# Optimization experiments

Measured on AMD Instinct MI355X. Metric: run time of the kernel, lower is better.

The kernel has to match this reference:

```python
import jax, jax.numpy as jnp
import numpy as np

LAMBDA_COORD = 5.0
LAMBDA_OBJ = 1.0
LAMBDA_NOOBJ = 0.5
LAMBDA_CLS = 1.0
EPS = 1e-07

B, N, M, NUM_CLASSES = 32, 25200, 200, 80


def setup_inputs() -> dict:
    key = jax.random.key(0)
    k1, k2, k3, k4, k5 = jax.random.split(key, 5)
    pred_bbox = jax.random.normal(k1, (B, N, 4), dtype=jnp.float32)
    pred_obj = jax.random.normal(k2, (B, N), dtype=jnp.float32)
    pred_cls = jax.random.normal(k3, (B, N, NUM_CLASSES), dtype=jnp.float32)
    gt_boxes = jax.random.uniform(k4, (B, M, 4), dtype=jnp.float32)
    gt_labels = jax.random.randint(k5, (B, M), 0, NUM_CLASSES, dtype=jnp.int64 if jax.config.jax_enable_x64 else jnp.int32)
    return {"pred_bbox": pred_bbox, "pred_obj": pred_obj, "pred_cls": pred_cls,
            "gt_boxes": gt_boxes, "gt_labels": gt_labels}


def _corners(boxes):
    # boxes: [..., 4] in (cx, cy, w, h)
    cx, cy, w, h = boxes[..., 0], boxes[..., 1], boxes[..., 2], boxes[..., 3]
    return cx - w / 2, cy - h / 2, cx + w / 2, cy + h / 2


def giou_loss(pred_boxes, target_boxes):
    px1, py1, px2, py2 = _corners(pred_boxes)
    tx1, ty1, tx2, ty2 = _corners(target_boxes)
    ix1 = jnp.maximum(px1, tx1)
    iy1 = jnp.maximum(py1, ty1)
    ix2 = jnp.minimum(px2, tx2)
    iy2 = jnp.minimum(py2, ty2)
    inter = jnp.clip(ix2 - ix1, 0) * jnp.clip(iy2 - iy1, 0)
    union = (px2 - px1) * (py2 - py1) + (tx2 - tx1) * (ty2 - ty1) - inter
    iou = inter / (union + EPS)
    ex1 = jnp.minimum(px1, tx1)
    ey1 = jnp.minimum(py1, ty1)
    ex2 = jnp.maximum(px2, tx2)
    ey2 = jnp.maximum(py2, ty2)
    enclose = (ex2 - ex1) * (ey2 - ey1)
    return 1.0 - (iou - (enclose - union) / (enclose + EPS))


def reference(pred_bbox, pred_obj, pred_cls, gt_boxes, gt_labels):
    m = gt_boxes.shape[1]  # obj_mask[b,:m] = True (static), anchor n < m matches gt n
    # bbox GIoU loss over positives
    loss_bbox = giou_loss(pred_bbox[:, :m], gt_boxes).mean() * LAMBDA_COORD
    # objectness BCE-with-logits: positives target 1, negatives target 0
    pos_logits = pred_obj[:, :m]
    neg_logits = pred_obj[:, m:]
    loss_obj_pos = jnp.mean(jax.nn.softplus(-pos_logits)) * LAMBDA_OBJ
    loss_obj_neg = jnp.mean(jax.nn.softplus(neg_logits)) * LAMBDA_NOOBJ
    loss_obj = loss_obj_pos + loss_obj_neg
    # classification cross-entropy over positives
    logits = pred_cls[:, :m]                       # [B, M, C]
    logp = jax.nn.log_softmax(logits, axis=-1)
    nll = -jnp.take_along_axis(logp, gt_labels[..., None].astype(jnp.int32), axis=-1)[..., 0]
    loss_cls = nll.mean() * LAMBDA_CLS
    total = loss_bbox + loss_obj + loss_cls
    # [detection_loss, bbox_loss, obj_loss, cls_loss]
    return jnp.stack([total, loss_bbox, loss_obj, loss_cls])
```

## Files before the change

kernel.cpp:

```cpp
#include <hip/hip_runtime.h>

#define BB 32
#define NN 25200
#define MM 200
#define CC 80

constexpr float EPSF = 1e-7f;
constexpr float L_COORD = 5.0f;
constexpr float L_NOOBJ = 0.5f;

constexpr int ITEMS_GIOU = BB * MM;
constexpr int ITEMS_CLS  = BB * MM;
constexpr int ITEMS_OBJ  = BB * NN;
constexpr int ITEMS_TOTAL = ITEMS_GIOU + ITEMS_CLS + ITEMS_OBJ;

constexpr int BLOCK = 256;
constexpr int GRID  = 1024;

__device__ __forceinline__ float softplus_f(float x) {
    return fmaxf(x, 0.0f) + log1pf(expf(-fabsf(x)));
}

__global__ __launch_bounds__(BLOCK)
void detloss_kernel(const float* __restrict__ pred_bbox,
                    const float* __restrict__ pred_obj,
                    const float* __restrict__ pred_cls,
                    const float* __restrict__ gt_boxes,
                    const int*   __restrict__ gt_labels,
                    float* __restrict__ out,
                    float* __restrict__ ws)
{
    float s_bbox = 0.0f, s_obj = 0.0f, s_cls = 0.0f;

    const int stride = GRID * BLOCK;
    for (int i = blockIdx.x * BLOCK + threadIdx.x; i < ITEMS_TOTAL; i += stride) {
        if (i < ITEMS_GIOU) {
            const int b = i / MM, m = i - b * MM;
            const float4 p = *(const float4*)(pred_bbox + ((size_t)b * NN + m) * 4);
            const float4 t = *(const float4*)(gt_boxes + (size_t)i * 4);
            const float px1 = p.x - p.z * 0.5f, py1 = p.y - p.w * 0.5f;
            const float px2 = p.x + p.z * 0.5f, py2 = p.y + p.w * 0.5f;
            const float tx1 = t.x - t.z * 0.5f, ty1 = t.y - t.w * 0.5f;
            const float tx2 = t.x + t.z * 0.5f, ty2 = t.y + t.w * 0.5f;
            const float ix1 = fmaxf(px1, tx1), iy1 = fmaxf(py1, ty1);
            const float ix2 = fminf(px2, tx2), iy2 = fminf(py2, ty2);
            const float inter = fmaxf(ix2 - ix1, 0.0f) * fmaxf(iy2 - iy1, 0.0f);
            const float uni = (px2 - px1) * (py2 - py1)
                            + (tx2 - tx1) * (ty2 - ty1) - inter;
            const float iou = inter / (uni + EPSF);
            const float ex1 = fminf(px1, tx1), ey1 = fminf(py1, ty1);
            const float ex2 = fmaxf(px2, tx2), ey2 = fmaxf(py2, ty2);
            const float enc = (ex2 - ex1) * (ey2 - ey1);
            s_bbox += 1.0f - (iou - (enc - uni) / (enc + EPSF));
        } else if (i < ITEMS_GIOU + ITEMS_CLS) {
            const int r = i - ITEMS_GIOU;
            const int b = r / MM, m = r - b * MM;
            const float* row = pred_cls + ((size_t)b * NN + m) * CC;
            float mx = -INFINITY;
            float v[CC];
            #pragma unroll 4
            for (int c = 0; c < CC; ++c) { v[c] = row[c]; mx = fmaxf(mx, v[c]); }
            float se = 0.0f;
            #pragma unroll 4
            for (int c = 0; c < CC; ++c) se += expf(v[c] - mx);
            const float lse = mx + logf(se);
            const int lbl = gt_labels[r];
            s_cls += lse - v[lbl];
        } else {
            const int e = i - (ITEMS_GIOU + ITEMS_CLS);
            const int n = e % NN;
            const float x = pred_obj[e];
            if (n < MM) s_obj += softplus_f(-x) * (1.0f / (float)(BB * MM));
            else        s_obj += softplus_f(x) * (L_NOOBJ / (float)(BB * (NN - MM)));
        }
    }

    #pragma unroll
    for (int off = 32; off > 0; off >>= 1) {
        s_bbox += __shfl_down(s_bbox, off, 64);
        s_obj  += __shfl_down(s_obj,  off, 64);
        s_cls  += __shfl_down(s_cls,  off, 64);
    }

    __shared__ float red[3][BLOCK / 64];
    const int wave = threadIdx.x >> 6;
    const int lane = threadIdx.x & 63;
    if (lane == 0) {
        red[0][wave] = s_bbox;
        red[1][wave] = s_obj;
        red[2][wave] = s_cls;
    }
    __syncthreads();

    if (threadIdx.x == 0) {
        float tb = 0.0f, to = 0.0f, tc = 0.0f;
        #pragma unroll
        for (int w = 0; w < BLOCK / 64; ++w) {
            tb += red[0][w]; to += red[1][w]; tc += red[2][w];
        }
        atomicAdd(&ws[0], tb);
        atomicAdd(&ws[1], to);
        atomicAdd(&ws[2], tc);
        __threadfence();
        const unsigned ticket = atomicAdd((unsigned*)&ws[3], 1u);
        if (ticket == (unsigned)(gridDim.x - 1)) {
            const float sb = atomicAdd(&ws[0], 0.0f);
            const float so = atomicAdd(&ws[1], 0.0f);
            const float sc = atomicAdd(&ws[2], 0.0f);
            const float loss_bbox = sb * (L_COORD / (float)(BB * MM));
            const float loss_obj  = so;
            const float loss_cls  = sc * (1.0f / (float)(BB * MM));
            out[0] = loss_bbox + loss_obj + loss_cls;
            out[1] = loss_bbox;
            out[2] = loss_obj;
            out[3] = loss_cls;
        }
    }
}

extern "C" void kernel_launch(void* const* d_in, const int* in_sizes, int n_in,
                              void* d_out, int out_size, void* d_ws, size_t ws_size,
                              hipStream_t stream) {
    const float* pred_bbox = (const float*)d_in[0];
    const float* pred_obj  = (const float*)d_in[1];
    const float* pred_cls  = (const float*)d_in[2];
    const float* gt_boxes  = (const float*)d_in[3];
    const int*   gt_labels = (const int*)d_in[4];
    float* out = (float*)d_out;
    float* ws  = (float*)d_ws;

    hipMemsetAsync(ws, 0, 4 * sizeof(float), stream);
    detloss_kernel<<<GRID, BLOCK, 0, stream>>>(pred_bbox, pred_obj, pred_cls,
                                               gt_boxes, gt_labels, out, ws);
}
```

Measured before the change: 365.9 us.

## Split class rows across 16 lanes, vectorize objectness loads, two-pass reduction

```diff
diff --git a/kernel.cpp b/kernel.cpp
--- a/kernel.cpp
+++ b/kernel.cpp
@@ -7,34 +7,34 @@
 
 constexpr float EPSF = 1e-7f;
 constexpr float L_COORD = 5.0f;
-constexpr float L_NOOBJ = 0.5f;
-
-constexpr int ITEMS_GIOU = BB * MM;
-constexpr int ITEMS_CLS  = BB * MM;
-constexpr int ITEMS_OBJ  = BB * NN;
-constexpr int ITEMS_TOTAL = ITEMS_GIOU + ITEMS_CLS + ITEMS_OBJ;
 
 constexpr int BLOCK = 256;
 constexpr int GRID  = 1024;
 
+constexpr int R_GIOU = BB * MM;
+constexpr int R_CLS  = R_GIOU + BB * MM * 16;
+constexpr int R_OBJ  = R_CLS + (BB * NN) / 4;
+
+constexpr float W_POS = 1.0f / (float)(BB * MM);
+constexpr float W_NEG = 0.5f / (float)(BB * (NN - MM));
+
 __device__ __forceinline__ float softplus_f(float x) {
-    return fmaxf(x, 0.0f) + log1pf(expf(-fabsf(x)));
+    return fmaxf(x, 0.0f) + __logf(1.0f + __expf(-fabsf(x)));
 }
 
 __global__ __launch_bounds__(BLOCK)
-void detloss_kernel(const float* __restrict__ pred_bbox,
-                    const float* __restrict__ pred_obj,
-                    const float* __restrict__ pred_cls,
-                    const float* __restrict__ gt_boxes,
-                    const int*   __restrict__ gt_labels,
-                    float* __restrict__ out,
-                    float* __restrict__ ws)
+void detloss_partials(const float* __restrict__ pred_bbox,
+                      const float* __restrict__ pred_obj,
+                      const float* __restrict__ pred_cls,
+                      const float* __restrict__ gt_boxes,
+                      const int*   __restrict__ gt_labels,
+                      float* __restrict__ ws)
 {
     float s_bbox = 0.0f, s_obj = 0.0f, s_cls = 0.0f;
 
     const int stride = GRID * BLOCK;
-    for (int i = blockIdx.x * BLOCK + threadIdx.x; i < ITEMS_TOTAL; i += stride) {
-        if (i < ITEMS_GIOU) {
+    for (int i = blockIdx.x * BLOCK + threadIdx.x; i < R_OBJ; i += stride) {
+        if (i < R_GIOU) {
             const int b = i / MM, m = i - b * MM;
             const float4 p = *(const float4*)(pred_bbox + ((size_t)b * NN + m) * 4);
             const float4 t = *(const float4*)(gt_boxes + (size_t)i * 4);
@@ -52,26 +52,43 @@
             const float ex2 = fmaxf(px2, tx2), ey2 = fmaxf(py2, ty2);
             const float enc = (ex2 - ex1) * (ey2 - ey1);
             s_bbox += 1.0f - (iou - (enc - uni) / (enc + EPSF));
-        } else if (i < ITEMS_GIOU + ITEMS_CLS) {
-            const int r = i - ITEMS_GIOU;
+        } else if (i < R_CLS) {
+            const int q   = i - R_GIOU;
+            const int r   = q >> 4;
+            const int sub = q & 15;
             const int b = r / MM, m = r - b * MM;
             const float* row = pred_cls + ((size_t)b * NN + m) * CC;
-            float mx = -INFINITY;
-            float v[CC];
-            #pragma unroll 4
-            for (int c = 0; c < CC; ++c) { v[c] = row[c]; mx = fmaxf(mx, v[c]); }
-            float se = 0.0f;
-            #pragma unroll 4
-            for (int c = 0; c < CC; ++c) se += expf(v[c] - mx);
-            const float lse = mx + logf(se);
-            const int lbl = gt_labels[r];
-            s_cls += lse - v[lbl];
+            float v0 = row[sub];
+            float v1 = row[sub + 16];
+            float v2 = row[sub + 32];
+            float v3 = row[sub + 48];
+            float v4 = row[sub + 64];
+            float mx = fmaxf(fmaxf(fmaxf(v0, v1), fmaxf(v2, v3)), v4);
+            #pragma unroll
+            for (int off = 1; off < 16; off <<= 1)
+                mx = fmaxf(mx, __shfl_xor(mx, off, 16));
+            float se = __expf(v0 - mx) + __expf(v1 - mx) + __expf(v2 - mx)
+                     + __expf(v3 - mx) + __expf(v4 - mx);
+            #pragma unroll
+            for (int off = 1; off < 16; off <<= 1)
+                se += __shfl_xor(se, off, 16);
+            if (sub == 0) {
+                const float lse = mx + __logf(se);
+                const int lbl = gt_labels[r];
+                s_cls += lse - row[lbl];
+            }
         } else {
-            const int e = i - (ITEMS_GIOU + ITEMS_CLS);
+            const int o = i - R_CLS;
+            const int e = o * 4;
             const int n = e % NN;
-            const float x = pred_obj[e];
-            if (n < MM) s_obj += softplus_f(-x) * (1.0f / (float)(BB * MM));
-            else        s_obj += softplus_f(x) * (L_NOOBJ / (float)(BB * (NN - MM)));
+            const float4 x = *(const float4*)(pred_obj + e);
+            if (n < MM) {
+                s_obj += W_POS * (softplus_f(-x.x) + softplus_f(-x.y)
+                                + softplus_f(-x.z) + softplus_f(-x.w));
+            } else {
+                s_obj += W_NEG * (softplus_f(x.x) + softplus_f(x.y)
+                                + softplus_f(x.z) + softplus_f(x.w));
+            }
         }
     }
 
@@ -98,23 +115,44 @@
         for (int w = 0; w < BLOCK / 64; ++w) {
             tb += red[0][w]; to += red[1][w]; tc += red[2][w];
         }
-        atomicAdd(&ws[0], tb);
-        atomicAdd(&ws[1], to);
-        atomicAdd(&ws[2], tc);
-        __threadfence();
-        const unsigned ticket = atomicAdd((unsigned*)&ws[3], 1u);
-        if (ticket == (unsigned)(gridDim.x - 1)) {
-            const float sb = atomicAdd(&ws[0], 0.0f);
-            const float so = atomicAdd(&ws[1], 0.0f);
-            const float sc = atomicAdd(&ws[2], 0.0f);
-            const float loss_bbox = sb * (L_COORD / (float)(BB * MM));
-            const float loss_obj  = so;
-            const float loss_cls  = sc * (1.0f / (float)(BB * MM));
-            out[0] = loss_bbox + loss_obj + loss_cls;
-            out[1] = loss_bbox;
-            out[2] = loss_obj;
-            out[3] = loss_cls;
+        ws[blockIdx.x]            = tb;
+        ws[GRID + blockIdx.x]     = to;
+        ws[2 * GRID + blockIdx.x] = tc;
+    }
+}
+
+__global__ __launch_bounds__(BLOCK)
+void detloss_finalize(const float* __restrict__ ws, float* __restrict__ out) {
+    float tb = 0.0f, to = 0.0f, tc = 0.0f;
+    for (int p = threadIdx.x; p < GRID; p += BLOCK) {
+        tb += ws[p];
+        to += ws[GRID + p];
+        tc += ws[2 * GRID + p];
+    }
+    #pragma unroll
+    for (int off = 32; off > 0; off >>= 1) {
+        tb += __shfl_down(tb, off, 64);
+        to += __shfl_down(to, off, 64);
+        tc += __shfl_down(tc, off, 64);
+    }
+    __shared__ float red[3][BLOCK / 64];
+    const int wave = threadIdx.x >> 6;
+    const int lane = threadIdx.x & 63;
+    if (lane == 0) { red[0][wave] = tb; red[1][wave] = to; red[2][wave] = tc; }
+    __syncthreads();
+    if (threadIdx.x == 0) {
+        float sb = 0.0f, so = 0.0f, sc = 0.0f;
+        #pragma unroll
+        for (int w = 0; w < BLOCK / 64; ++w) {
+            sb += red[0][w]; so += red[1][w]; sc += red[2][w];
         }
+        const float loss_bbox = sb * (L_COORD / (float)(BB * MM));
+        const float loss_obj  = so;
+        const float loss_cls  = sc * (1.0f / (float)(BB * MM));
+        out[0] = loss_bbox + loss_obj + loss_cls;
+        out[1] = loss_bbox;
+        out[2] = loss_obj;
+        out[3] = loss_cls;
     }
 }
 
@@ -129,7 +167,7 @@
     float* out = (float*)d_out;
     float* ws  = (float*)d_ws;
 
-    hipMemsetAsync(ws, 0, 4 * sizeof(float), stream);
-    detloss_kernel<<<GRID, BLOCK, 0, stream>>>(pred_bbox, pred_obj, pred_cls,
-                                               gt_boxes, gt_labels, out, ws);
+    detloss_partials<<<GRID, BLOCK, 0, stream>>>(pred_bbox, pred_obj, pred_cls,
+                                                 gt_boxes, gt_labels, ws);
+    detloss_finalize<<<1, BLOCK, 0, stream>>>(ws, out);
 }
```

Result: faster. 295.6 us (-19.2%).
